# Optimization experiments

Measured on AMD Instinct MI355X. Metric: run time of the kernel, lower is better.

The kernel has to match this reference:

```python
import jax, jax.numpy as jnp
import numpy as np

WEIGHT_BIT = 8
QMAX = 2 ** (WEIGHT_BIT - 1) - 1   # 127
QMIN = -2 ** (WEIGHT_BIT - 1)      # -128


def fake_quant_per_channel(W):
    # IBERT symmetric per-output-channel quantization of the weight matrix.
    # W: [out_features, in_features]; scale per output channel.
    max_abs = jnp.max(jnp.abs(W), axis=1, keepdims=True)
    scale = jnp.maximum(max_abs, 1e-8) / QMAX
    w_int = jnp.clip(jnp.round(W / scale), QMIN, QMAX)
    return w_int * scale


def setup_inputs() -> dict:
    key = jax.random.key(0)
    k1, k2, k3, k4 = jax.random.split(key, 4)
    B, S, D_FF, D = 16, 1024, 4096, 1024
    hidden_states = jax.random.normal(k1, (B, S, D_FF), dtype=jnp.float32)
    input_tensor = jax.random.normal(k2, (B, S, D), dtype=jnp.float32)
    W = jax.random.normal(k3, (D, D_FF), dtype=jnp.float32) * 0.02
    b = jax.random.normal(k4, (D,), dtype=jnp.float32) * 0.02
    return {"hidden_states": hidden_states, "input_tensor": input_tensor, "W": W, "b": b}


def reference(hidden_states, input_tensor, W, b):
    # QuantLinear: fake-quantized (8-bit per-channel symmetric) weight GEMM + bias.
    w_fq = fake_quant_per_channel(W)
    out = jnp.einsum("bsf,df->bsd", hidden_states, w_fq) + b  # [B, S, D]
    # dropout p=0.0 (inference) -> identity; residual add
    return out + input_tensor
```

## Files before the change

kernel.cpp:

```cpp
#include <hip/hip_runtime.h>
#include <hip/hip_bf16.h>
#include <stdint.h>


#define M_TOTAL 16384
#define KDIM    4096
#define NDIM    1024
#define BM      256
#define BN      256
#define BK      64
#define NT      (KDIM / BK)
#define BUF_BYTES 65536
#define B_OFF   32768

using f32x4  = __attribute__((ext_vector_type(4))) float;
using bf16x8 = __attribute__((ext_vector_type(8))) __bf16;
using u16x8  = __attribute__((ext_vector_type(8))) unsigned short;

__device__ __forceinline__ unsigned short f32_to_bf16_bits(float f) {
  union { float f; uint32_t u; } x; x.f = f;
  uint32_t r = x.u + 0x7FFFu + ((x.u >> 16) & 1u);
  return (unsigned short)(r >> 16);
}

__device__ __forceinline__ void async_copy16(const void* g, void* l) {
  __builtin_amdgcn_global_load_lds(
      (const __attribute__((address_space(1))) void*)g,
      (__attribute__((address_space(3))) void*)l,
      16, 0, 0);
}

__global__ __launch_bounds__(256) void quantize_w_kernel(
    const float* __restrict__ W, unsigned short* __restrict__ Bq) {
  const int row = blockIdx.x;
  const int t   = threadIdx.x;
  const f32x4* wv = (const f32x4*)(W + (size_t)row * KDIM);

  f32x4 v[4];
  float m = 0.0f;
#pragma unroll
  for (int i = 0; i < 4; ++i) {
    v[i] = wv[t * 4 + i];
#pragma unroll
    for (int j = 0; j < 4; ++j) m = fmaxf(m, fabsf(v[i][j]));
  }
#pragma unroll
  for (int off = 32; off >= 1; off >>= 1) m = fmaxf(m, __shfl_xor(m, off));
  __shared__ float smax[4];
  if ((t & 63) == 0) smax[t >> 6] = m;
  __syncthreads();
  m = fmaxf(fmaxf(smax[0], smax[1]), fmaxf(smax[2], smax[3]));

  const float scale = fmaxf(m, 1e-8f) / 127.0f;

  u16x8 o[2];
#pragma unroll
  for (int i = 0; i < 16; ++i) {
    float w = v[i >> 2][i & 3];
    float q = rintf(w / scale);
    q = fminf(127.0f, fmaxf(-128.0f, q));
    o[i >> 3][i & 7] = f32_to_bf16_bits(q * scale);
  }
  u16x8* dst = (u16x8*)(Bq + (size_t)row * KDIM + t * 16);
  dst[0] = o[0];
  dst[1] = o[1];
}

__global__ __launch_bounds__(256) void cast_hidden_kernel(
    const float* __restrict__ A, unsigned short* __restrict__ Ab, int n8) {
  const int stride = gridDim.x * blockDim.x;
  for (int i = blockIdx.x * blockDim.x + threadIdx.x; i < n8; i += stride) {
    const f32x4* src = (const f32x4*)A + (size_t)i * 2;
    f32x4 a = src[0], b = src[1];
    u16x8 o;
#pragma unroll
    for (int j = 0; j < 4; ++j) o[j]     = f32_to_bf16_bits(a[j]);
#pragma unroll
    for (int j = 0; j < 4; ++j) o[4 + j] = f32_to_bf16_bits(b[j]);
    ((u16x8*)Ab)[i] = o;
  }
}

__global__ __launch_bounds__(512, 2) void gemm_8phase_kernel(
    const unsigned short* __restrict__ A,
    const unsigned short* __restrict__ Bq,
    const float* __restrict__ bias,
    const float* __restrict__ res,
    float* __restrict__ out) {
  __shared__ char smem[2 * BUF_BYTES];

  const int nwg = (M_TOTAL / BM) * (NDIM / BN);
  int bid = blockIdx.x;
  bid = (bid & 7) * (nwg >> 3) + (bid >> 3);
  const int nb = bid & 3;
  const int mb = bid >> 2;
  const int m0 = mb * BM, n0 = nb * BN;

  const int tid  = threadIdx.x;
  const int lane = tid & 63;
  const int wid  = tid >> 6;
  const int wm   = wid >> 2;
  const int wn   = wid & 3;

  const int srow  = lane >> 3;
  const int scol8 = (lane & 7) ^ (srow & 7);
  const unsigned short* agp[4];
  const unsigned short* bgp[4];
#pragma unroll
  for (int i = 0; i < 4; ++i) {
    agp[i] = A  + (size_t)(m0 + i * 64 + wid * 8 + srow) * KDIM + scol8 * 8;
    bgp[i] = Bq + (size_t)(n0 + i * 64 + wid * 8 + srow) * KDIM + scol8 * 8;
  }

#define STAGE(BUFBASE, K0) do {                                              \
    _Pragma("unroll")                                                        \
    for (int i_ = 0; i_ < 4; ++i_) {                                         \
      async_copy16(agp[i_] + (K0), (BUFBASE) + (i_ * 64 + wid * 8) * 128);   \
      async_copy16(bgp[i_] + (K0), (BUFBASE) + B_OFF + (i_ * 64 + wid * 8) * 128); \
    }                                                                        \
  } while (0)

  const int fr = lane & 15;
  const int kg = lane >> 4;
  const int cs0 = ((kg)     ^ (fr & 7)) * 16;
  const int cs1 = ((kg + 4) ^ (fr & 7)) * 16;
  const int baseA = (wm * 128 + fr) * 128;
  const int baseB = B_OFF + (wn * 64 + fr) * 128;

  f32x4 acc[8][4];
  const f32x4 zero = {0.f, 0.f, 0.f, 0.f};
#pragma unroll
  for (int i = 0; i < 8; ++i)
#pragma unroll
    for (int j = 0; j < 4; ++j) acc[i][j] = zero;

#define LDA4(MB, CS) do {                                                    \
    _Pragma("unroll")                                                        \
    for (int q_ = 0; q_ < 4; ++q_)                                           \
      a[q_] = *(const bf16x8*)(cur + baseA + ((MB) + q_) * 2048 + (CS));     \
  } while (0)
#define LDB4(CS) do {                                                        \
    _Pragma("unroll")                                                        \
    for (int q_ = 0; q_ < 4; ++q_)                                           \
      b[q_] = *(const bf16x8*)(cur + baseB + q_ * 2048 + (CS));              \
  } while (0)
#define MFMA16(MB) do {                                                      \
    __builtin_amdgcn_s_setprio(1);                                           \
    _Pragma("unroll")                                                        \
    for (int mi_ = 0; mi_ < 4; ++mi_)                                        \
      _Pragma("unroll")                                                      \
      for (int nj_ = 0; nj_ < 4; ++nj_)                                      \
        acc[(MB) + mi_][nj_] = __builtin_amdgcn_mfma_f32_16x16x32_bf16(      \
            a[mi_], b[nj_], acc[(MB) + mi_][nj_], 0, 0, 0);                  \
    __builtin_amdgcn_s_setprio(0);                                           \
  } while (0)

  STAGE(smem, 0);
  asm volatile("s_waitcnt vmcnt(0)" ::: "memory");
  __builtin_amdgcn_s_barrier();

  for (int tt = 0; tt < NT; ++tt) {
    char* cur = smem + (tt & 1) * BUF_BYTES;
    char* nxt = smem + ((tt + 1) & 1) * BUF_BYTES;
    bf16x8 a[4], b[4];

    if (tt + 1 < NT) STAGE(nxt, (tt + 1) * BK);
    LDA4(0, cs0); LDB4(cs0);
    MFMA16(0);
    __builtin_amdgcn_s_barrier();

    LDA4(4, cs0);
    MFMA16(4);
    __builtin_amdgcn_s_barrier();

    LDA4(0, cs1); LDB4(cs1);
    MFMA16(0);
    __builtin_amdgcn_s_barrier();

    LDA4(4, cs1);
    MFMA16(4);
    asm volatile("s_waitcnt vmcnt(0)" ::: "memory");
    __builtin_amdgcn_s_barrier();
  }

  const int col = lane & 15;
  const int rg  = (lane >> 4) * 4;
#pragma unroll
  for (int nj = 0; nj < 4; ++nj) {
    const int d = n0 + wn * 64 + nj * 16 + col;
    const float bb = bias[d];
#pragma unroll
    for (int mi = 0; mi < 8; ++mi) {
      const int mrow = m0 + wm * 128 + mi * 16 + rg;
#pragma unroll
      for (int r = 0; r < 4; ++r) {
        const size_t idx = (size_t)(mrow + r) * NDIM + d;
        out[idx] = acc[mi][nj][r] + bb + res[idx];
      }
    }
  }
#undef STAGE
#undef LDA4
#undef LDB4
#undef MFMA16
}

extern "C" void kernel_launch(void* const* d_in, const int* in_sizes, int n_in,
                              void* d_out, int out_size, void* d_ws, size_t ws_size,
                              hipStream_t stream) {
  const float* hidden = (const float*)d_in[0];
  const float* resid  = (const float*)d_in[1];
  const float* W      = (const float*)d_in[2];
  const float* bias   = (const float*)d_in[3];
  float* out          = (float*)d_out;

  unsigned short* Abf = (unsigned short*)d_ws;
  unsigned short* Bq  = Abf + (size_t)M_TOTAL * KDIM;

  quantize_w_kernel<<<NDIM, 256, 0, stream>>>(W, Bq);
  cast_hidden_kernel<<<2048, 256, 0, stream>>>(hidden, Abf, (M_TOTAL * KDIM) / 8);
  gemm_8phase_kernel<<<(M_TOTAL / BM) * (NDIM / BN), 512, 0, stream>>>(Abf, Bq, bias, resid, out);
}
```

Measured before the change: 574.0 us.

## Split next-tile async prefetch into four chunks interleaved across MFMA phases

Splits the single per-iteration global-to-LDS prefetch into four chunks (two B halves, two A halves). Each chunk is issued in a different MFMA phase, so memory traffic is spread through the K-loop instead of bursting at its start. Uses vmcnt(2) partial waits so the last A chunk can still be in flight across the iteration boundary, since the next iteration's first phase only reads rows from the other A chunk. Adds an extra barrier per phase between the LDS fragment reads and the MFMAs, which costs synchronisation and relies on careful ordering of which rows each chunk covers.

```diff
diff --git a/kernel.cpp b/kernel.cpp
--- a/kernel.cpp
+++ b/kernel.cpp
@@ -99,8 +99,10 @@
   const int tid  = threadIdx.x;
   const int lane = tid & 63;
   const int wid  = tid >> 6;
-  const int wm   = wid >> 2;
+  const int wm   = wid >> 1;
+  const int wmm  = wid >> 2;
   const int wn   = wid & 3;
+  (void)wm;
 
   const int srow  = lane >> 3;
   const int scol8 = (lane & 7) ^ (srow & 7);
@@ -112,19 +114,20 @@
     bgp[i] = Bq + (size_t)(n0 + i * 64 + wid * 8 + srow) * KDIM + scol8 * 8;
   }
 
-#define STAGE(BUFBASE, K0) do {                                              \
-    _Pragma("unroll")                                                        \
-    for (int i_ = 0; i_ < 4; ++i_) {                                         \
-      async_copy16(agp[i_] + (K0), (BUFBASE) + (i_ * 64 + wid * 8) * 128);   \
-      async_copy16(bgp[i_] + (K0), (BUFBASE) + B_OFF + (i_ * 64 + wid * 8) * 128); \
-    }                                                                        \
-  } while (0)
+#define STG_B1(BUF, K0) do { async_copy16(bgp[0] + (K0), (BUF) + B_OFF + (0 * 64 + wid * 8) * 128); \
+                             async_copy16(bgp[1] + (K0), (BUF) + B_OFF + (1 * 64 + wid * 8) * 128); } while (0)
+#define STG_B2(BUF, K0) do { async_copy16(bgp[2] + (K0), (BUF) + B_OFF + (2 * 64 + wid * 8) * 128); \
+                             async_copy16(bgp[3] + (K0), (BUF) + B_OFF + (3 * 64 + wid * 8) * 128); } while (0)
+#define STG_A1(BUF, K0) do { async_copy16(agp[0] + (K0), (BUF) + (0 * 64 + wid * 8) * 128); \
+                             async_copy16(agp[2] + (K0), (BUF) + (2 * 64 + wid * 8) * 128); } while (0)
+#define STG_A2(BUF, K0) do { async_copy16(agp[1] + (K0), (BUF) + (1 * 64 + wid * 8) * 128); \
+                             async_copy16(agp[3] + (K0), (BUF) + (3 * 64 + wid * 8) * 128); } while (0)
 
   const int fr = lane & 15;
   const int kg = lane >> 4;
   const int cs0 = ((kg)     ^ (fr & 7)) * 16;
   const int cs1 = ((kg + 4) ^ (fr & 7)) * 16;
-  const int baseA = (wm * 128 + fr) * 128;
+  const int baseA = (wmm * 128 + fr) * 128;
   const int baseB = B_OFF + (wn * 64 + fr) * 128;
 
   f32x4 acc[8][4];
@@ -154,33 +157,46 @@
             a[mi_], b[nj_], acc[(MB) + mi_][nj_], 0, 0, 0);                  \
     __builtin_amdgcn_s_setprio(0);                                           \
   } while (0)
-
-  STAGE(smem, 0);
-  asm volatile("s_waitcnt vmcnt(0)" ::: "memory");
-  __builtin_amdgcn_s_barrier();
+#define BAR()    __builtin_amdgcn_s_barrier()
+#define VMCNT2() asm volatile("s_waitcnt vmcnt(2)" ::: "memory")
+#define VMCNT0() asm volatile("s_waitcnt vmcnt(0)" ::: "memory")
+
+  STG_B1(smem, 0); STG_B2(smem, 0); STG_A1(smem, 0); STG_A2(smem, 0);
+  VMCNT0();
+  BAR();
 
   for (int tt = 0; tt < NT; ++tt) {
     char* cur = smem + (tt & 1) * BUF_BYTES;
     char* nxt = smem + ((tt + 1) & 1) * BUF_BYTES;
+    const int k1 = (tt + 1) * BK;
+    const bool pf = (tt + 1 < NT);
     bf16x8 a[4], b[4];
 
-    if (tt + 1 < NT) STAGE(nxt, (tt + 1) * BK);
     LDA4(0, cs0); LDB4(cs0);
+    if (pf) STG_B1(nxt, k1);
+    BAR();
     MFMA16(0);
-    __builtin_amdgcn_s_barrier();
+    if (pf) VMCNT2(); else VMCNT0();
+    BAR();
 
     LDA4(4, cs0);
+    if (pf) STG_B2(nxt, k1);
+    BAR();
     MFMA16(4);
-    __builtin_amdgcn_s_barrier();
+    BAR();
 
     LDA4(0, cs1); LDB4(cs1);
+    if (pf) STG_A1(nxt, k1);
+    BAR();
     MFMA16(0);
-    __builtin_amdgcn_s_barrier();
+    BAR();
 
     LDA4(4, cs1);
+    if (pf) STG_A2(nxt, k1);
+    BAR();
     MFMA16(4);
-    asm volatile("s_waitcnt vmcnt(0)" ::: "memory");
-    __builtin_amdgcn_s_barrier();
+    VMCNT2();
+    BAR();
   }
 
   const int col = lane & 15;
@@ -191,7 +207,7 @@
     const float bb = bias[d];
 #pragma unroll
     for (int mi = 0; mi < 8; ++mi) {
-      const int mrow = m0 + wm * 128 + mi * 16 + rg;
+      const int mrow = m0 + wmm * 128 + mi * 16 + rg;
 #pragma unroll
       for (int r = 0; r < 4; ++r) {
         const size_t idx = (size_t)(mrow + r) * NDIM + d;
@@ -199,10 +215,16 @@
       }
     }
   }
-#undef STAGE
+#undef STG_B1
+#undef STG_B2
+#undef STG_A1
+#undef STG_A2
 #undef LDA4
 #undef LDB4
 #undef MFMA16
+#undef BAR
+#undef VMCNT2
+#undef VMCNT0
 }
 
 extern "C" void kernel_launch(void* const* d_in, const int* in_sizes, int n_in,
```

New measurement: 558.6 us. 1.03x faster.
